# Kernel tuning notes

Hardware: AMD Instinct MI355X
Metric: run time of the kernel (lower is better)

Reference implementation:

```python
import jax, jax.numpy as jnp
import numpy as np

NUM_USERS = 30000
NUM_ITEMS = 30000
N = NUM_USERS + NUM_ITEMS          # total graph nodes (users + items)
E = 800000                          # number of edges
EMBED_K = 64
INTENTS = 4
D = EMBED_K // INTENTS              # per-intent channel chunk
N_LAYERS = 1
ROUTING_ITERS = 2


def setup_inputs() -> dict:
    key = jax.random.key(0)
    k1, k2, k3, k4 = jax.random.split(key, 4)
    Gu = jax.random.normal(k1, (NUM_USERS, EMBED_K), jnp.float32) * 0.1
    Gi = jax.random.normal(k2, (NUM_ITEMS, EMBED_K), jnp.float32) * 0.1
    # head list: guarantee every node appears at least once as a head so that
    # D = 1/sqrt(row_degree) is finite (real CF graphs have no isolated rows)
    edge_h = jnp.concatenate([jnp.arange(N, dtype=jnp.int64),
                              jax.random.randint(k3, (E - N,), 0, N, dtype=jnp.int64)])
    edge_t = jax.random.randint(k4, (E,), 0, N, dtype=jnp.int64)
    return {"Gu": Gu, "Gi": Gi, "edge_h": edge_h, "edge_t": edge_t}


def _l2norm(x, eps=1e-12):
    # matches torch.nn.functional.normalize(dim=-1)
    return x / jnp.sqrt(jnp.maximum(jnp.sum(x * x, axis=-1, keepdims=True), eps))


def reference(Gu, Gi, edge_h, edge_t):
    ego = jnp.concatenate([Gu, Gi], axis=0)            # [N, K]
    all_emb = [ego]
    # routing attention logits per intent per edge (initialized to ones)
    A_values = jnp.ones((INTENTS, E), dtype=Gu.dtype)
    for _ in range(N_LAYERS):
        # split embed dim into INTENTS contiguous chunks -> [I, N, D]
        X = ego.reshape(N, INTENTS, D).transpose(1, 0, 2)
        Z = X
        for _t in range(ROUTING_ITERS):
            # softmax over intents per edge (pick=False path; p_train is always False)
            scores = jax.nn.softmax(A_values, axis=0)                    # [I, E]
            # per-intent row degrees (sparse.sum over dim=1 indexes rows = heads)
            deg = jnp.zeros((INTENTS, N), scores.dtype).at[:, edge_h].add(scores)
            d_col = 1.0 / jnp.sqrt(deg)                                  # [I, N]
            # D_col @ X, A @ (.), D_col @ (.)  -- note original applies D_col twice (as written)
            Y = d_col[..., None] * X                                     # [I, N, D]
            msg = scores[..., None] * Y[:, edge_t, :]                    # [I, E, D]
            Z = jnp.zeros((INTENTS, N, D), X.dtype).at[:, edge_h, :].add(msg)
            Z = d_col[..., None] * Z                                     # [I, N, D]
            # attention update: normalize(head) . tanh(normalize(tail))
            head = _l2norm(Z[:, edge_h, :])                              # [I, E, D]
            tail = _l2norm(X[:, edge_t, :])                              # [I, E, D]
            A_values = A_values + jnp.sum(head * jnp.tanh(tail), axis=-1)
        # concat intent chunks back along channel dim
        ego = Z.transpose(1, 0, 2).reshape(N, EMBED_K)
        all_emb.append(ego)
    out = jnp.mean(jnp.stack(all_emb, axis=1), axis=1)   # [N, K]
    return out[:NUM_USERS], out[NUM_USERS:]
```

## Files before the change

### kernel.cpp

```cpp
#include <hip/hip_runtime.h>
#include <hip/hip_fp16.h>


#define NUSERS 30000
#define NN     60000
#define EE     800000
#define SCAN_B ((NN + 255) / 256)
#define EV_B   ((EE / 4 + 255) / 256)
#define NW1_B  ((NN + 1 + 3) / 4)
#define N8_B   (NN / 8)

__device__ __forceinline__ float getX(const float* __restrict__ Gu,
                                      const float* __restrict__ Gi,
                                      int n, int c) {
    return (n < NUSERS) ? Gu[n * 64 + c] : Gi[(n - NUSERS) * 64 + c];
}

__device__ __forceinline__ int clampN(int n) {
    return ((unsigned)n < (unsigned)NN) ? n : 0;
}

__device__ __forceinline__ __half2 bch2(float f) {
    return __builtin_bit_cast(__half2, f);
}


__global__ void edge_count(const int* __restrict__ eh, int* __restrict__ deg0,
                           int* __restrict__ rank) {
    int e4 = (blockIdx.x * blockDim.x + threadIdx.x) * 4;
    if (e4 >= EE) return;
    int4 h = *(const int4*)(eh + e4);
    int4 r;
    r.x = atomicAdd(&deg0[clampN(h.x)], 1);
    r.y = atomicAdd(&deg0[clampN(h.y)], 1);
    r.z = atomicAdd(&deg0[clampN(h.z)], 1);
    r.w = atomicAdd(&deg0[clampN(h.w)], 1);
    *(int4*)(rank + e4) = r;
}

__global__ void scan_local(const int* __restrict__ deg0, int* __restrict__ offsets,
                           int* __restrict__ bsum) {
    int gid = blockIdx.x * 256 + threadIdx.x;
    int lane = threadIdx.x & 63, w = threadIdx.x >> 6;
    int vdeg = (gid < NN) ? deg0[gid] : 0;
    int x = vdeg;
    #pragma unroll
    for (int d = 1; d < 64; d <<= 1) {
        int y = __shfl_up(x, d, 64);
        if (lane >= d) x += y;
    }
    __shared__ int wsum[4];
    if (lane == 63) wsum[w] = x;
    __syncthreads();
    int wpre = 0;
    #pragma unroll
    for (int j = 0; j < 4; ++j) wpre += (j < w) ? wsum[j] : 0;
    int incl = x + wpre;
    if (gid < NN) offsets[gid] = incl - vdeg;
    if (threadIdx.x == 255) bsum[blockIdx.x] = incl;
}

__global__ void scan_add2(int* __restrict__ offsets, const int* __restrict__ bsum) {
    int tid = threadIdx.x, lane = tid & 63, w = tid >> 6;
    int vv = (tid < SCAN_B) ? bsum[tid] : 0;
    int x = vv;
    #pragma unroll
    for (int d = 1; d < 64; d <<= 1) {
        int y = __shfl_up(x, d, 64);
        if (lane >= d) x += y;
    }
    __shared__ int wsum[4];
    __shared__ int bpre;
    if (lane == 63) wsum[w] = x;
    __syncthreads();
    int wpre = 0;
    #pragma unroll
    for (int j = 0; j < 4; ++j) wpre += (j < w) ? wsum[j] : 0;
    if (tid == blockIdx.x) bpre = x + wpre - vv;
    __syncthreads();
    int gid = blockIdx.x * 256 + tid;
    if (gid < NN) offsets[gid] += bpre;
    if (gid == 0) offsets[NN] = EE;
}

__global__ void scatter_prep(const int* __restrict__ eh, const int* __restrict__ et,
                             const int* __restrict__ rank,
                             const int* __restrict__ offsets,
                             int* __restrict__ csr_tail,
                             const float* __restrict__ Gu, const float* __restrict__ Gi,
                             const int* __restrict__ deg0,
                             __half* __restrict__ Ytab, __half* __restrict__ Ttab) {
    if (blockIdx.x < EV_B) {
        int e4 = (blockIdx.x * 256 + threadIdx.x) * 4;
        if (e4 >= EE) return;
        int4 h = *(const int4*)(eh + e4);
        int4 t = *(const int4*)(et + e4);
        int4 r = *(const int4*)(rank + e4);
        int s0 = offsets[clampN(h.x)] + r.x;
        if ((unsigned)s0 < EE) csr_tail[s0] = clampN(t.x);
        int s1 = offsets[clampN(h.y)] + r.y;
        if ((unsigned)s1 < EE) csr_tail[s1] = clampN(t.y);
        int s2 = offsets[clampN(h.z)] + r.z;
        if ((unsigned)s2 < EE) csr_tail[s2] = clampN(t.z);
        int s3 = offsets[clampN(h.w)] + r.w;
        if ((unsigned)s3 < EE) csr_tail[s3] = clampN(t.w);
    } else {
        int n = (blockIdx.x - EV_B) * 4 + (threadIdx.x >> 6);
        if (n > NN) return;
        int lane = threadIdx.x & 63;
        float x = (n < NN) ? getX(Gu, Gi, n, lane) : 0.f;
        float sx = x * x;
        #pragma unroll
        for (int m = 1; m < 16; m <<= 1) sx += __shfl_xor(sx, m, 64);
        float invx = rsqrtf(fmaxf(sx, 1e-12f));
        float d0 = rsqrtf(fmaxf(0.25f * (float)((n < NN) ? deg0[n] : 1), 1e-30f));
        size_t a = (size_t)n * 64 + lane;
        Ytab[a] = __float2half(d0 * x);
        Ttab[a] = __float2half(tanhf(x * invx));
    }
}

__global__ void zat(const int* __restrict__ offsets, const int* __restrict__ csr_tail,
                    const __half* __restrict__ Ytab, const __half* __restrict__ Ttab,
                    __half* __restrict__ s4, float* __restrict__ dcol1,
                    const float* __restrict__ Gu, const float* __restrict__ Gi,
                    __half* __restrict__ Y1i) {
    __shared__ __half zn[8][72];
    __shared__ float ssum[8][4];
    __shared__ int soff[9];
    int tid = threadIdx.x;
    int n0 = blockIdx.x * 8;
    if (tid < 9) soff[tid] = offsets[n0 + tid];
    if (tid >= 32 && tid < 64) ssum[(tid - 32) >> 2][tid & 3] = 0.f;
    __syncthreads();

    {
        int g = tid >> 5, cc = tid & 31;
        int s0 = soff[g], s1 = soff[g + 1];
        float accx = 0.f, accy = 0.f;
        for (int base = s0; base < s1; base += 4) {
            #pragma unroll
            for (int u = 0; u < 4; ++u) {
                int kk = base + u;
                bool act = kk < s1;
                int kc = act ? kk : s0;
                int t = act ? csr_tail[kc] : NN;
                __half2 y = *(const __half2*)(Ytab + (size_t)t * 64 + cc * 2);
                float2 yf = __half22float2(y);
                accx += yf.x; accy += yf.y;
            }
        }
        float ss = accx * accx + accy * accy;
        ss += __shfl_xor(ss, 1, 64);
        ss += __shfl_xor(ss, 2, 64);
        ss += __shfl_xor(ss, 4, 64);
        float inv = rsqrtf(fmaxf(ss, 1e-12f));
        *(__half2*)&zn[g][cc * 2] = __floats2half2_rn(accx * inv, accy * inv);
    }
    __syncthreads();

    int e0 = soff[0], e1 = soff[8];
    for (int k = e0 + tid; k < e1; k += 256) {
        int hl = 0;
        #pragma unroll
        for (int j = 1; j < 8; ++j) hl += (k >= soff[j]) ? 1 : 0;
        int t = csr_tail[k];
        const float4* tp = (const float4*)(Ttab + (size_t)t * 64);
        float dot[4];
        #pragma unroll
        for (int i = 0; i < 4; ++i) {
            float4 za = *(const float4*)&zn[hl][i * 16];
            float4 zb = *(const float4*)&zn[hl][i * 16 + 8];
            float4 ta = tp[2 * i], tb = tp[2 * i + 1];
            __half2 acc = __floats2half2_rn(0.f, 0.f);
            acc = __hfma2(bch2(za.x), bch2(ta.x), acc);
            acc = __hfma2(bch2(za.y), bch2(ta.y), acc);
            acc = __hfma2(bch2(za.z), bch2(ta.z), acc);
            acc = __hfma2(bch2(za.w), bch2(ta.w), acc);
            acc = __hfma2(bch2(zb.x), bch2(tb.x), acc);
            acc = __hfma2(bch2(zb.y), bch2(tb.y), acc);
            acc = __hfma2(bch2(zb.z), bch2(tb.z), acc);
            acc = __hfma2(bch2(zb.w), bch2(tb.w), acc);
            float2 f = __half22float2(acc);
            dot[i] = f.x + f.y;
        }
        float mx = fmaxf(fmaxf(dot[0], dot[1]), fmaxf(dot[2], dot[3]));
        float q0 = __expf(dot[0] - mx), q1 = __expf(dot[1] - mx);
        float q2 = __expf(dot[2] - mx), q3 = __expf(dot[3] - mx);
        float inv = 1.f / (q0 + q1 + q2 + q3);
        q0 *= inv; q1 *= inv; q2 *= inv; q3 *= inv;
        __half2 o01 = __floats2half2_rn(q0, q1);
        __half2 o23 = __floats2half2_rn(q2, q3);
        int2 st;
        st.x = __builtin_bit_cast(int, o01);
        st.y = __builtin_bit_cast(int, o23);
        *(int2*)(s4 + (size_t)k * 4) = st;
        atomicAdd(&ssum[hl][0], q0);
        atomicAdd(&ssum[hl][1], q1);
        atomicAdd(&ssum[hl][2], q2);
        atomicAdd(&ssum[hl][3], q3);
    }
    __syncthreads();

    if (tid < 32) {
        int nn = n0 + (tid >> 2);
        dcol1[nn * 4 + (tid & 3)] = rsqrtf(fmaxf(ssum[tid >> 2][tid & 3], 1e-30f));
    }
    #pragma unroll
    for (int v = tid; v < 512; v += 256) {
        int nn = n0 + (v >> 6);
        int ch = v & 63;
        float d = rsqrtf(fmaxf(ssum[v >> 6][ch >> 4], 1e-30f));
        float x = getX(Gu, Gi, nn, ch);
        Y1i[(size_t)nn * 64 + ch] = __float2half(d * x);
    }
}

__global__ void outk(const int* __restrict__ offsets, const int* __restrict__ csr_tail,
                     const __half* __restrict__ Y1i, const __half* __restrict__ s4,
                     const float* __restrict__ dcol1,
                     const float* __restrict__ Gu, const float* __restrict__ Gi,
                     float* __restrict__ out) {
    int tid = threadIdx.x;
    int n = blockIdx.x * 8 + (tid >> 5);
    if (n >= NN) return;
    int cc = tid & 31;
    int s0 = offsets[n], s1 = offsets[n + 1];
    float accx = 0.f, accy = 0.f;
    for (int base = s0; base < s1; base += 4) {
        #pragma unroll
        for (int u = 0; u < 4; ++u) {
            int kk = base + u;
            bool act = kk < s1;
            int kc = act ? kk : s0;
            int t = csr_tail[kc];
            int2 raw = *(const int2*)(s4 + (size_t)kc * 4);
            int word = (cc & 16) ? raw.y : raw.x;
            unsigned short us = (unsigned short)(word >> ((cc & 8) ? 16 : 0));
            float s = act ? __half2float(__builtin_bit_cast(__half, us)) : 0.f;
            __half2 y = *(const __half2*)(Y1i + (size_t)t * 64 + cc * 2);
            float2 yf = __half22float2(y);
            accx = fmaf(s, yf.x, accx);
            accy = fmaf(s, yf.y, accy);
        }
    }
    float d = dcol1[n * 4 + (cc >> 3)];
    int ch = cc * 2;
    const float* xr = (n < NUSERS) ? (Gu + (size_t)n * 64 + ch)
                                   : (Gi + (size_t)(n - NUSERS) * 64 + ch);
    float2 x2 = *(const float2*)xr;
    float2 o;
    o.x = 0.5f * (x2.x + d * accx);
    o.y = 0.5f * (x2.y + d * accy);
    *(float2*)(out + (size_t)n * 64 + ch) = o;
}


extern "C" void kernel_launch(void* const* d_in, const int* in_sizes, int n_in,
                              void* d_out, int out_size, void* d_ws, size_t ws_size,
                              hipStream_t stream) {
    const float* Gu = (const float*)d_in[0];
    const float* Gi = (const float*)d_in[1];
    const int* eh = (const int*)d_in[2];
    const int* et = (const int*)d_in[3];
    float* out = (float*)d_out;

    char* p = (char*)d_ws;
    __half* s4       = (__half*)p;     p += (size_t)EE * 4 * 2;
    int*    csr_tail = (int*)p;        p += (size_t)EE * 4;
    int*    rank     = (int*)p;        p += (size_t)EE * 4;
    int*    offsets  = (int*)p;        p += ((size_t)(NN + 1) * 4 + 15) / 16 * 16;
    int*    deg0     = (int*)p;        p += (size_t)NN * 4;
    int*    bsum     = (int*)p;        p += ((size_t)SCAN_B * 4 + 15) / 16 * 16;
    float*  dcol1    = (float*)p;      p += (size_t)NN * 4 * 4;
    __half* Ytab     = (__half*)p;     p += (size_t)(NN + 1) * 64 * 2;
    __half* Ttab     = (__half*)p;     p += (size_t)(NN + 1) * 64 * 2;
    __half* Y1i      = (__half*)p;

    hipMemsetAsync(deg0, 0, NN * sizeof(int), stream);
    edge_count<<<EV_B, 256, 0, stream>>>(eh, deg0, rank);
    scan_local<<<SCAN_B, 256, 0, stream>>>(deg0, offsets, bsum);
    scan_add2<<<SCAN_B, 256, 0, stream>>>(offsets, bsum);

    scatter_prep<<<EV_B + NW1_B, 256, 0, stream>>>(eh, et, rank, offsets, csr_tail,
                                                   Gu, Gi, deg0, Ytab, Ttab);

    zat<<<N8_B, 256, 0, stream>>>(offsets, csr_tail, Ytab, Ttab, s4, dcol1,
                                  Gu, Gi, Y1i);

    outk<<<N8_B, 256, 0, stream>>>(offsets, csr_tail, Y1i, s4, dcol1, Gu, Gi, out);
}
```

Before: 237.2 us.

## Move node-table prep into the count kernel and apply degree scales at gather time

Node-side precompute (half-precision X and tanh(normalized X) tables) now runs in the same launch as the edge-degree atomics, leaving the scatter kernel to handle edges only. Degree normalizers become separate per-node float arrays: d0 is computed in the scan kernel and dcol1 is applied per gathered neighbor in outk. This removes the Y1i table write in zat and the dependence of node prep on the scan. The cost is an extra scalar gather per edge (d0a[t] in zat, dcol1[t] in outk) in the hot gather loops.

Result: no change. 234.9 us (median of 3 runs) (-1.0%).

```diff
diff --git a/kernel.cpp b/kernel.cpp
--- a/kernel.cpp
+++ b/kernel.cpp
@@ -24,86 +24,20 @@
     return __builtin_bit_cast(__half2, f);
 }
 
-
-__global__ void edge_count(const int* __restrict__ eh, int* __restrict__ deg0,
-                           int* __restrict__ rank) {
-    int e4 = (blockIdx.x * blockDim.x + threadIdx.x) * 4;
-    if (e4 >= EE) return;
-    int4 h = *(const int4*)(eh + e4);
-    int4 r;
-    r.x = atomicAdd(&deg0[clampN(h.x)], 1);
-    r.y = atomicAdd(&deg0[clampN(h.y)], 1);
-    r.z = atomicAdd(&deg0[clampN(h.z)], 1);
-    r.w = atomicAdd(&deg0[clampN(h.w)], 1);
-    *(int4*)(rank + e4) = r;
-}
-
-__global__ void scan_local(const int* __restrict__ deg0, int* __restrict__ offsets,
-                           int* __restrict__ bsum) {
-    int gid = blockIdx.x * 256 + threadIdx.x;
-    int lane = threadIdx.x & 63, w = threadIdx.x >> 6;
-    int vdeg = (gid < NN) ? deg0[gid] : 0;
-    int x = vdeg;
-    #pragma unroll
-    for (int d = 1; d < 64; d <<= 1) {
-        int y = __shfl_up(x, d, 64);
-        if (lane >= d) x += y;
-    }
-    __shared__ int wsum[4];
-    if (lane == 63) wsum[w] = x;
-    __syncthreads();
-    int wpre = 0;
-    #pragma unroll
-    for (int j = 0; j < 4; ++j) wpre += (j < w) ? wsum[j] : 0;
-    int incl = x + wpre;
-    if (gid < NN) offsets[gid] = incl - vdeg;
-    if (threadIdx.x == 255) bsum[blockIdx.x] = incl;
-}
-
-__global__ void scan_add2(int* __restrict__ offsets, const int* __restrict__ bsum) {
-    int tid = threadIdx.x, lane = tid & 63, w = tid >> 6;
-    int vv = (tid < SCAN_B) ? bsum[tid] : 0;
-    int x = vv;
-    #pragma unroll
-    for (int d = 1; d < 64; d <<= 1) {
-        int y = __shfl_up(x, d, 64);
-        if (lane >= d) x += y;
-    }
-    __shared__ int wsum[4];
-    __shared__ int bpre;
-    if (lane == 63) wsum[w] = x;
-    __syncthreads();
-    int wpre = 0;
-    #pragma unroll
-    for (int j = 0; j < 4; ++j) wpre += (j < w) ? wsum[j] : 0;
-    if (tid == blockIdx.x) bpre = x + wpre - vv;
-    __syncthreads();
-    int gid = blockIdx.x * 256 + tid;
-    if (gid < NN) offsets[gid] += bpre;
-    if (gid == 0) offsets[NN] = EE;
-}
-
-__global__ void scatter_prep(const int* __restrict__ eh, const int* __restrict__ et,
-                             const int* __restrict__ rank,
-                             const int* __restrict__ offsets,
-                             int* __restrict__ csr_tail,
-                             const float* __restrict__ Gu, const float* __restrict__ Gi,
-                             const int* __restrict__ deg0,
-                             __half* __restrict__ Ytab, __half* __restrict__ Ttab) {
+__global__ void count_prep(const int* __restrict__ eh, int* __restrict__ deg0,
+                           int* __restrict__ rank,
+                           const float* __restrict__ Gu, const float* __restrict__ Gi,
+                           __half* __restrict__ Xh, __half* __restrict__ Ttab) {
     if (blockIdx.x < EV_B) {
         int e4 = (blockIdx.x * 256 + threadIdx.x) * 4;
         if (e4 >= EE) return;
         int4 h = *(const int4*)(eh + e4);
-        int4 t = *(const int4*)(et + e4);
-        int4 r = *(const int4*)(rank + e4);
-        int s0 = offsets[clampN(h.x)] + r.x;
-        if ((unsigned)s0 < EE) csr_tail[s0] = clampN(t.x);
-        int s1 = offsets[clampN(h.y)] + r.y;
-        if ((unsigned)s1 < EE) csr_tail[s1] = clampN(t.y);
-        int s2 = offsets[clampN(h.z)] + r.z;
-        if ((unsigned)s2 < EE) csr_tail[s2] = clampN(t.z);
-        int s3 = offsets[clampN(h.w)] + r.w;
-        if ((unsigned)s3 < EE) csr_tail[s3] = clampN(t.w);
+        int4 r;
+        r.x = atomicAdd(&deg0[clampN(h.x)], 1);
+        r.y = atomicAdd(&deg0[clampN(h.y)], 1);
+        r.z = atomicAdd(&deg0[clampN(h.z)], 1);
+        r.w = atomicAdd(&deg0[clampN(h.w)], 1);
+        *(int4*)(rank + e4) = r;
     } else {
         int n = (blockIdx.x - EV_B) * 4 + (threadIdx.x >> 6);
         if (n > NN) return;
@@ -113,18 +47,81 @@
         #pragma unroll
         for (int m = 1; m < 16; m <<= 1) sx += __shfl_xor(sx, m, 64);
         float invx = rsqrtf(fmaxf(sx, 1e-12f));
-        float d0 = rsqrtf(fmaxf(0.25f * (float)((n < NN) ? deg0[n] : 1), 1e-30f));
         size_t a = (size_t)n * 64 + lane;
-        Ytab[a] = __float2half(d0 * x);
+        Xh[a]   = __float2half(x);
         Ttab[a] = __float2half(tanhf(x * invx));
     }
 }
 
+__global__ void scan_local(const int* __restrict__ deg0, int* __restrict__ offsets,
+                           int* __restrict__ bsum, float* __restrict__ d0a) {
+    int gid = blockIdx.x * 256 + threadIdx.x;
+    int lane = threadIdx.x & 63, w = threadIdx.x >> 6;
+    int vdeg = (gid < NN) ? deg0[gid] : 0;
+    if (gid < NN) d0a[gid] = rsqrtf(fmaxf(0.25f * (float)vdeg, 1e-30f));
+    if (gid == NN) d0a[NN] = 0.f;
+    int x = vdeg;
+    #pragma unroll
+    for (int d = 1; d < 64; d <<= 1) {
+        int y = __shfl_up(x, d, 64);
+        if (lane >= d) x += y;
+    }
+    __shared__ int wsum[4];
+    if (lane == 63) wsum[w] = x;
+    __syncthreads();
+    int wpre = 0;
+    #pragma unroll
+    for (int j = 0; j < 4; ++j) wpre += (j < w) ? wsum[j] : 0;
+    int incl = x + wpre;
+    if (gid < NN) offsets[gid] = incl - vdeg;
+    if (threadIdx.x == 255) bsum[blockIdx.x] = incl;
+}
+
+__global__ void scan_add2(int* __restrict__ offsets, const int* __restrict__ bsum) {
+    int tid = threadIdx.x, lane = tid & 63, w = tid >> 6;
+    int vv = (tid < SCAN_B) ? bsum[tid] : 0;
+    int x = vv;
+    #pragma unroll
+    for (int d = 1; d < 64; d <<= 1) {
+        int y = __shfl_up(x, d, 64);
+        if (lane >= d) x += y;
+    }
+    __shared__ int wsum[4];
+    __shared__ int bpre;
+    if (lane == 63) wsum[w] = x;
+    __syncthreads();
+    int wpre = 0;
+    #pragma unroll
+    for (int j = 0; j < 4; ++j) wpre += (j < w) ? wsum[j] : 0;
+    if (tid == blockIdx.x) bpre = x + wpre - vv;
+    __syncthreads();
+    int gid = blockIdx.x * 256 + tid;
+    if (gid < NN) offsets[gid] += bpre;
+    if (gid == 0) offsets[NN] = EE;
+}
+
+__global__ void scatter(const int* __restrict__ eh, const int* __restrict__ et,
+                        const int* __restrict__ rank, const int* __restrict__ offsets,
+                        int* __restrict__ csr_tail) {
+    int e4 = (blockIdx.x * 256 + threadIdx.x) * 4;
+    if (e4 >= EE) return;
+    int4 h = *(const int4*)(eh + e4);
+    int4 t = *(const int4*)(et + e4);
+    int4 r = *(const int4*)(rank + e4);
+    int s0 = offsets[clampN(h.x)] + r.x;
+    if ((unsigned)s0 < EE) csr_tail[s0] = clampN(t.x);
+    int s1 = offsets[clampN(h.y)] + r.y;
+    if ((unsigned)s1 < EE) csr_tail[s1] = clampN(t.y);
+    int s2 = offsets[clampN(h.z)] + r.z;
+    if ((unsigned)s2 < EE) csr_tail[s2] = clampN(t.z);
+    int s3 = offsets[clampN(h.w)] + r.w;
+    if ((unsigned)s3 < EE) csr_tail[s3] = clampN(t.w);
+}
+
 __global__ void zat(const int* __restrict__ offsets, const int* __restrict__ csr_tail,
-                    const __half* __restrict__ Ytab, const __half* __restrict__ Ttab,
-                    __half* __restrict__ s4, float* __restrict__ dcol1,
-                    const float* __restrict__ Gu, const float* __restrict__ Gi,
-                    __half* __restrict__ Y1i) {
+                    const __half* __restrict__ Xh, const float* __restrict__ d0a,
+                    const __half* __restrict__ Ttab,
+                    __half* __restrict__ s4, float* __restrict__ dcol1) {
     __shared__ __half zn[8][72];
     __shared__ float ssum[8][4];
     __shared__ int soff[9];
@@ -145,9 +142,11 @@
                 bool act = kk < s1;
                 int kc = act ? kk : s0;
                 int t = act ? csr_tail[kc] : NN;
-                __half2 y = *(const __half2*)(Ytab + (size_t)t * 64 + cc * 2);
+                float d0v = d0a[t];
+                __half2 y = *(const __half2*)(Xh + (size_t)t * 64 + cc * 2);
                 float2 yf = __half22float2(y);
-                accx += yf.x; accy += yf.y;
+                accx = fmaf(d0v, yf.x, accx);
+                accy = fmaf(d0v, yf.y, accy);
             }
         }
         float ss = accx * accx + accy * accy;
@@ -206,18 +205,10 @@
         int nn = n0 + (tid >> 2);
         dcol1[nn * 4 + (tid & 3)] = rsqrtf(fmaxf(ssum[tid >> 2][tid & 3], 1e-30f));
     }
-    #pragma unroll
-    for (int v = tid; v < 512; v += 256) {
-        int nn = n0 + (v >> 6);
-        int ch = v & 63;
-        float d = rsqrtf(fmaxf(ssum[v >> 6][ch >> 4], 1e-30f));
-        float x = getX(Gu, Gi, nn, ch);
-        Y1i[(size_t)nn * 64 + ch] = __float2half(d * x);
-    }
 }
 
 __global__ void outk(const int* __restrict__ offsets, const int* __restrict__ csr_tail,
-                     const __half* __restrict__ Y1i, const __half* __restrict__ s4,
+                     const __half* __restrict__ Xh, const __half* __restrict__ s4,
                      const float* __restrict__ dcol1,
                      const float* __restrict__ Gu, const float* __restrict__ Gi,
                      float* __restrict__ out) {
@@ -225,6 +216,7 @@
     int n = blockIdx.x * 8 + (tid >> 5);
     if (n >= NN) return;
     int cc = tid & 31;
+    int i = cc >> 3;
     int s0 = offsets[n], s1 = offsets[n + 1];
     float accx = 0.f, accy = 0.f;
     for (int base = s0; base < s1; base += 4) {
@@ -238,13 +230,14 @@
             int word = (cc & 16) ? raw.y : raw.x;
             unsigned short us = (unsigned short)(word >> ((cc & 8) ? 16 : 0));
             float s = act ? __half2float(__builtin_bit_cast(__half, us)) : 0.f;
-            __half2 y = *(const __half2*)(Y1i + (size_t)t * 64 + cc * 2);
+            float w = s * dcol1[t * 4 + i];
+            __half2 y = *(const __half2*)(Xh + (size_t)t * 64 + cc * 2);
             float2 yf = __half22float2(y);
-            accx = fmaf(s, yf.x, accx);
-            accy = fmaf(s, yf.y, accy);
+            accx = fmaf(w, yf.x, accx);
+            accy = fmaf(w, yf.y, accy);
         }
     }
-    float d = dcol1[n * 4 + (cc >> 3)];
+    float d = dcol1[n * 4 + i];
     int ch = cc * 2;
     const float* xr = (n < NUSERS) ? (Gu + (size_t)n * 64 + ch)
                                    : (Gi + (size_t)(n - NUSERS) * 64 + ch);
@@ -273,20 +266,18 @@
     int*    deg0     = (int*)p;        p += (size_t)NN * 4;
     int*    bsum     = (int*)p;        p += ((size_t)SCAN_B * 4 + 15) / 16 * 16;
     float*  dcol1    = (float*)p;      p += (size_t)NN * 4 * 4;
-    __half* Ytab     = (__half*)p;     p += (size_t)(NN + 1) * 64 * 2;
-    __half* Ttab     = (__half*)p;     p += (size_t)(NN + 1) * 64 * 2;
-    __half* Y1i      = (__half*)p;
+    float*  d0a      = (float*)p;      p += ((size_t)(NN + 1) * 4 + 15) / 16 * 16;
+    __half* Xh       = (__half*)p;     p += (size_t)(NN + 1) * 64 * 2;
+    __half* Ttab     = (__half*)p;
 
     hipMemsetAsync(deg0, 0, NN * sizeof(int), stream);
-    edge_count<<<EV_B, 256, 0, stream>>>(eh, deg0, rank);
-    scan_local<<<SCAN_B, 256, 0, stream>>>(deg0, offsets, bsum);
+    count_prep<<<EV_B + NW1_B, 256, 0, stream>>>(eh, deg0, rank, Gu, Gi, Xh, Ttab);
+    scan_local<<<SCAN_B, 256, 0, stream>>>(deg0, offsets, bsum, d0a);
     scan_add2<<<SCAN_B, 256, 0, stream>>>(offsets, bsum);
 
-    scatter_prep<<<EV_B + NW1_B, 256, 0, stream>>>(eh, et, rank, offsets, csr_tail,
-                                                   Gu, Gi, deg0, Ytab, Ttab);
-
-    zat<<<N8_B, 256, 0, stream>>>(offsets, csr_tail, Ytab, Ttab, s4, dcol1,
-                                  Gu, Gi, Y1i);
-
-    outk<<<N8_B, 256, 0, stream>>>(offsets, csr_tail, Y1i, s4, dcol1, Gu, Gi, out);
-}
+    scatter<<<EV_B, 256, 0, stream>>>(eh, et, rank, offsets, csr_tail);
+
+    zat<<<N8_B, 256, 0, stream>>>(offsets, csr_tail, Xh, d0a, Ttab, s4, dcol1);
+
+    outk<<<N8_B, 256, 0, stream>>>(offsets, csr_tail, Xh, s4, dcol1, Gu, Gi, out);
+}
```
